# Performance work log

Measured on AMD Instinct MI355X. Metric: run time of the kernel, lower is better.

## Reference

```python
import jax, jax.numpy as jnp
import numpy as np

B, S, X = 4, 1024, 1024
C, D = 8, 2          # num_channels, coordinate_dim
WIDTH, DEPTH = 16, 4


def setup_inputs() -> dict:
    key = jax.random.key(0)
    ks = jax.random.split(key, 8)
    scale = 1.0 / np.sqrt(WIDTH)
    return {
        "yu": jax.random.normal(ks[0], (B, S, C + D), dtype=jnp.float32),
        "x": jax.random.normal(ks[1], (B, X, D), dtype=jnp.float32),
        "W_in": jax.random.normal(ks[2], (1, WIDTH), dtype=jnp.float32),
        "b_in": jax.random.normal(ks[3], (WIDTH,), dtype=jnp.float32) * 0.1,
        "W_hid": jax.random.normal(ks[4], (DEPTH, WIDTH, WIDTH), dtype=jnp.float32) * scale,
        "b_hid": jax.random.normal(ks[5], (DEPTH, WIDTH), dtype=jnp.float32) * 0.1,
        "W_out": jax.random.normal(ks[6], (WIDTH, 1), dtype=jnp.float32) * scale,
        "b_out": jax.random.normal(ks[7], (1,), dtype=jnp.float32) * 0.1,
    }


def reference(yu, x, W_in, b_in, W_hid, b_hid, W_out, b_out):
    # split sensor positions y and sensor values u
    y = yu[:, :, -D:]           # (B, S, D)
    u = yu[:, :, :C]            # (B, S, C)
    # pairwise squared distances between eval points x and sensors y
    diff = x[:, None, :, :] - y[:, :, None, :]   # (B, S, X, D)
    r = jnp.sum(diff * diff, axis=-1)            # (B, S, X)
    # DeepResidualNetwork(1 -> 1): Linear, DEPTH x [tanh(Linear)+skip], Linear
    h = r[..., None] * W_in[0] + b_in            # (B, S, X, WIDTH)

    def res_layer(h, wb):
        w, b = wb
        return jnp.tanh(h @ w + b) + h, None

    h, _ = jax.lax.scan(res_layer, h, (W_hid, b_hid))
    k = jnp.squeeze(h @ W_out, -1) + b_out[0]    # (B, S, X)
    # Monte-Carlo integral over sensors
    return jnp.einsum('bsx,bsc->bxc', k, u) / S  # (B, X, C)
```

## Files before the change

kernel.cpp:

```cpp
#include <hip/hip_runtime.h>
#include <math.h>

#define BB 4
#define SS 1024
#define XX 1024
#define CC 8
#define DD 2
#define WIDTH 16
#define DEPTH 4

#define NLUT 8192
#define RSCALE 32.0f

__device__ __forceinline__ float fast_tanh(float v) {
    float ax = __builtin_fabsf(v);
    float e  = __builtin_amdgcn_exp2f(ax * -2.885390081777927f);
    float t  = fmaf(2.0f, __builtin_amdgcn_rcpf(1.0f + e), -1.0f);
    return __builtin_copysignf(t, v);
}

__global__ __launch_bounds__(256) void build_lut(
    const float* __restrict__ W_in, const float* __restrict__ b_in,
    const float* __restrict__ W_hid, const float* __restrict__ b_hid,
    const float* __restrict__ W_out, const float* __restrict__ b_out,
    float* __restrict__ lut)
{
    const int idx = blockIdx.x * 256 + threadIdx.x;
    if (idx >= NLUT) return;
    const float r = (float)idx * (1.0f / RSCALE);

    float h[WIDTH];
#pragma unroll
    for (int j = 0; j < WIDTH; ++j) h[j] = fmaf(r, W_in[j], b_in[j]);

#pragma unroll
    for (int l = 0; l < DEPTH; ++l) {
        const float* W  = W_hid + l * WIDTH * WIDTH;
        const float* bb = b_hid + l * WIDTH;
        float pre[WIDTH];
#pragma unroll
        for (int j = 0; j < WIDTH; ++j) pre[j] = bb[j];
#pragma unroll
        for (int i = 0; i < WIDTH; ++i) {
            const float hi = h[i];
#pragma unroll
            for (int j = 0; j < WIDTH; ++j)
                pre[j] = fmaf(hi, W[i * WIDTH + j], pre[j]);
        }
#pragma unroll
        for (int j = 0; j < WIDTH; ++j) h[j] += fast_tanh(pre[j]);
    }

    float k = b_out[0];
#pragma unroll
    for (int j = 0; j < WIDTH; ++j) k = fmaf(h[j], W_out[j], k);
    lut[idx] = k;
}

__global__ __launch_bounds__(256) void ccl_main(
    const float* __restrict__ yu,
    const float* __restrict__ x,
    const float* __restrict__ lut_g,
    float* __restrict__ out)
{
    __shared__ float lut_s[NLUT];

    const int bx  = blockIdx.x;
    const int b   = bx >> 10;
    const int xi  = bx & (XX - 1);
    const int tid = threadIdx.x;

    {
        const float4* src = reinterpret_cast<const float4*>(lut_g);
        float4*       dst = reinterpret_cast<float4*>(lut_s);
#pragma unroll
        for (int i = 0; i < NLUT / 4 / 256; ++i)
            dst[tid + i * 256] = src[tid + i * 256];
    }

    const float px0 = x[((size_t)b * XX + xi) * DD + 0];
    const float px1 = x[((size_t)b * XX + xi) * DD + 1];
    const float* yub = yu + (size_t)b * SS * (CC + DD);

    __syncthreads();

    float acc[CC];
#pragma unroll
    for (int c = 0; c < CC; ++c) acc[c] = 0.0f;

#pragma unroll
    for (int t = 0; t < SS / 256; ++t) {
        const int s = tid + t * 256;
        const float2* row = reinterpret_cast<const float2*>(yub + (size_t)s * (CC + DD));
        float2 a0 = row[0], a1 = row[1], a2 = row[2], a3 = row[3], a4 = row[4];

        const float d0 = px0 - a4.x;
        const float d1 = px1 - a4.y;
        const float r  = fmaf(d0, d0, d1 * d1);

        float rf = r * RSCALE;
        int   i  = (int)rf;
        i = min(i, NLUT - 2);
        const float w  = rf - (float)i;
        const float f0 = lut_s[i];
        const float f1 = lut_s[i + 1];
        const float k  = fmaf(w, f1 - f0, f0);

        acc[0] = fmaf(k, a0.x, acc[0]);
        acc[1] = fmaf(k, a0.y, acc[1]);
        acc[2] = fmaf(k, a1.x, acc[2]);
        acc[3] = fmaf(k, a1.y, acc[3]);
        acc[4] = fmaf(k, a2.x, acc[4]);
        acc[5] = fmaf(k, a2.y, acc[5]);
        acc[6] = fmaf(k, a3.x, acc[6]);
        acc[7] = fmaf(k, a3.y, acc[7]);
    }

#pragma unroll
    for (int c = 0; c < CC; ++c) {
        float v = acc[c];
#pragma unroll
        for (int off = 32; off > 0; off >>= 1)
            v += __shfl_down(v, off, 64);
        acc[c] = v;
    }

    __syncthreads();
    const int lane = tid & 63;
    const int wv   = tid >> 6;
    if (lane == 0) {
#pragma unroll
        for (int c = 0; c < CC; ++c) lut_s[wv * CC + c] = acc[c];
    }
    __syncthreads();
    if (tid < CC) {
        const float v = lut_s[0 * CC + tid] + lut_s[1 * CC + tid] +
                        lut_s[2 * CC + tid] + lut_s[3 * CC + tid];
        out[((size_t)b * XX + xi) * CC + tid] = v * (1.0f / SS);
    }
}

extern "C" void kernel_launch(void* const* d_in, const int* in_sizes, int n_in,
                              void* d_out, int out_size, void* d_ws, size_t ws_size,
                              hipStream_t stream) {
    const float* yu    = (const float*)d_in[0];
    const float* x     = (const float*)d_in[1];
    const float* W_in  = (const float*)d_in[2];
    const float* b_in  = (const float*)d_in[3];
    const float* W_hid = (const float*)d_in[4];
    const float* b_hid = (const float*)d_in[5];
    const float* W_out = (const float*)d_in[6];
    const float* b_out = (const float*)d_in[7];
    float* out = (float*)d_out;
    float* lut = (float*)d_ws;

    build_lut<<<dim3(NLUT / 256), dim3(256), 0, stream>>>(
        W_in, b_in, W_hid, b_hid, W_out, b_out, lut);

    ccl_main<<<dim3(BB * XX), dim3(256), 0, stream>>>(yu, x, lut, out);
}
```

Measured before the change: 98.52 us.

## Process eight eval points per block, reusing LUT copy and sensor registers

Result: faster. 94.96 us (-3.6%).

```diff
diff --git a/kernel.cpp b/kernel.cpp
--- a/kernel.cpp
+++ b/kernel.cpp
@@ -11,6 +11,7 @@
 
 #define NLUT 8192
 #define RSCALE 32.0f
+#define GQ 8
 
 __device__ __forceinline__ float fast_tanh(float v) {
     float ax = __builtin_fabsf(v);
@@ -64,10 +65,11 @@
     float* __restrict__ out)
 {
     __shared__ float lut_s[NLUT];
+    __shared__ float red[4][CC];
 
     const int bx  = blockIdx.x;
-    const int b   = bx >> 10;
-    const int xi  = bx & (XX - 1);
+    const int b   = bx / (XX / GQ);
+    const int xi0 = (bx % (XX / GQ)) * GQ;
     const int tid = threadIdx.x;
 
     {
@@ -78,65 +80,72 @@
             dst[tid + i * 256] = src[tid + i * 256];
     }
 
-    const float px0 = x[((size_t)b * XX + xi) * DD + 0];
-    const float px1 = x[((size_t)b * XX + xi) * DD + 1];
     const float* yub = yu + (size_t)b * SS * (CC + DD);
+    float2 yp[4];
+    float  up[4][CC];
+#pragma unroll
+    for (int i = 0; i < 4; ++i) {
+        const int s = tid + i * 256;
+        const float2* row = reinterpret_cast<const float2*>(yub + (size_t)s * (CC + DD));
+        float2 a0 = row[0], a1 = row[1], a2 = row[2], a3 = row[3];
+        yp[i] = row[4];
+        up[i][0] = a0.x; up[i][1] = a0.y; up[i][2] = a1.x; up[i][3] = a1.y;
+        up[i][4] = a2.x; up[i][5] = a2.y; up[i][6] = a3.x; up[i][7] = a3.y;
+    }
+
+    const float* xp = x + ((size_t)b * XX + xi0) * DD;
 
     __syncthreads();
 
-    float acc[CC];
-#pragma unroll
-    for (int c = 0; c < CC; ++c) acc[c] = 0.0f;
+    const int lane = tid & 63;
+    const int wv   = tid >> 6;
 
 #pragma unroll
-    for (int t = 0; t < SS / 256; ++t) {
-        const int s = tid + t * 256;
-        const float2* row = reinterpret_cast<const float2*>(yub + (size_t)s * (CC + DD));
-        float2 a0 = row[0], a1 = row[1], a2 = row[2], a3 = row[3], a4 = row[4];
+    for (int q = 0; q < GQ; ++q) {
+        const float px0 = xp[2 * q + 0];
+        const float px1 = xp[2 * q + 1];
 
-        const float d0 = px0 - a4.x;
-        const float d1 = px1 - a4.y;
-        const float r  = fmaf(d0, d0, d1 * d1);
-
-        float rf = r * RSCALE;
-        int   i  = (int)rf;
-        i = min(i, NLUT - 2);
-        const float w  = rf - (float)i;
-        const float f0 = lut_s[i];
-        const float f1 = lut_s[i + 1];
-        const float k  = fmaf(w, f1 - f0, f0);
-
-        acc[0] = fmaf(k, a0.x, acc[0]);
-        acc[1] = fmaf(k, a0.y, acc[1]);
-        acc[2] = fmaf(k, a1.x, acc[2]);
-        acc[3] = fmaf(k, a1.y, acc[3]);
-        acc[4] = fmaf(k, a2.x, acc[4]);
-        acc[5] = fmaf(k, a2.y, acc[5]);
-        acc[6] = fmaf(k, a3.x, acc[6]);
-        acc[7] = fmaf(k, a3.y, acc[7]);
-    }
+        float acc[CC];
+#pragma unroll
+        for (int c = 0; c < CC; ++c) acc[c] = 0.0f;
 
 #pragma unroll
-    for (int c = 0; c < CC; ++c) {
-        float v = acc[c];
+        for (int i = 0; i < 4; ++i) {
+            const float d0 = px0 - yp[i].x;
+            const float d1 = px1 - yp[i].y;
+            const float r  = fmaf(d0, d0, d1 * d1);
+
+            float rf = r * RSCALE;
+            int   ix = (int)rf;
+            ix = min(ix, NLUT - 2);
+            const float w  = rf - (float)ix;
+            const float f0 = lut_s[ix];
+            const float f1 = lut_s[ix + 1];
+            const float k  = fmaf(w, f1 - f0, f0);
+
 #pragma unroll
-        for (int off = 32; off > 0; off >>= 1)
-            v += __shfl_down(v, off, 64);
-        acc[c] = v;
-    }
+            for (int c = 0; c < CC; ++c) acc[c] = fmaf(k, up[i][c], acc[c]);
+        }
 
-    __syncthreads();
-    const int lane = tid & 63;
-    const int wv   = tid >> 6;
-    if (lane == 0) {
 #pragma unroll
-        for (int c = 0; c < CC; ++c) lut_s[wv * CC + c] = acc[c];
-    }
-    __syncthreads();
-    if (tid < CC) {
-        const float v = lut_s[0 * CC + tid] + lut_s[1 * CC + tid] +
-                        lut_s[2 * CC + tid] + lut_s[3 * CC + tid];
-        out[((size_t)b * XX + xi) * CC + tid] = v * (1.0f / SS);
+        for (int c = 0; c < CC; ++c) {
+            float v = acc[c];
+#pragma unroll
+            for (int off = 32; off > 0; off >>= 1)
+                v += __shfl_down(v, off, 64);
+            acc[c] = v;
+        }
+
+        __syncthreads();
+        if (lane == 0) {
+#pragma unroll
+            for (int c = 0; c < CC; ++c) red[wv][c] = acc[c];
+        }
+        __syncthreads();
+        if (tid < CC) {
+            const float v = red[0][tid] + red[1][tid] + red[2][tid] + red[3][tid];
+            out[((size_t)b * XX + xi0 + q) * CC + tid] = v * (1.0f / SS);
+        }
     }
 }
 
@@ -157,5 +166,5 @@
     build_lut<<<dim3(NLUT / 256), dim3(256), 0, stream>>>(
         W_in, b_in, W_hid, b_hid, W_out, b_out, lut);
 
-    ccl_main<<<dim3(BB * XX), dim3(256), 0, stream>>>(yu, x, lut, out);
+    ccl_main<<<dim3(BB * XX / GQ), dim3(256), 0, stream>>>(yu, x, lut, out);
 }
```
